# Optimization experiments

Measured on AMD Instinct MI355X. Metric: run time of the kernel, lower is better.

Reference implementation:

```python
import jax, jax.numpy as jnp
import numpy as np

D_MODEL = 14
N_HEADS = 2
SINK_TEMP = 0.1
SINK_ITERS = 20
EPS = 1e-10


def setup_inputs() -> dict:
    key = jax.random.key(0)
    ks = jax.random.split(key, 12)
    b, n, d = 64, 1024, D_MODEL
    s = 1.0 / np.sqrt(d)
    return {
        "x": jax.random.normal(ks[0], (b, n, d), dtype=jnp.float32),
        "certainty": jax.random.uniform(ks[1], (b, n), dtype=jnp.float32),
        "permutation": jax.random.randint(ks[2], (b, n), 0, n).astype(jnp.int64),
        "Wq": jax.random.normal(ks[3], (d, d), dtype=jnp.float32) * s,
        "bq": jnp.zeros((d,), dtype=jnp.float32),
        "Wk": jax.random.normal(ks[4], (d, d), dtype=jnp.float32) * s,
        "bk": jnp.zeros((d,), dtype=jnp.float32),
        "Wv": jax.random.normal(ks[5], (d, d), dtype=jnp.float32) * s,
        "bv": jnp.zeros((d,), dtype=jnp.float32),
        "Wo": jax.random.normal(ks[6], (d, d), dtype=jnp.float32) * s,
        "bo": jnp.zeros((d,), dtype=jnp.float32),
    }


def _split_heads(t, b, n):
    # (b, n, d) -> (b, H, n, hd)
    return t.reshape(b, n, N_HEADS, D_MODEL // N_HEADS).transpose(0, 2, 1, 3)


def reference(x, certainty, permutation, Wq, bq, Wk, bk, Wv, bv, Wo, bo):
    b, n, d = x.shape
    hd = d // N_HEADS
    Q = _split_heads(x @ Wq.T + bq, b, n)
    K = _split_heads(x @ Wk.T + bk, b, n)
    V = _split_heads(x @ Wv.T + bv, b, n)
    scores = jnp.einsum("bhqd,bhkd->bhqk", Q, K) / jnp.sqrt(jnp.float32(hd))
    attn = jax.nn.softmax(scores, axis=-1)  # dropout is identity at eval
    out = jnp.einsum("bhqk,bhkd->bhqd", attn, V)
    out = out.transpose(0, 2, 1, 3).reshape(b, n, d)
    out = out @ Wo.T + bo

    avg_attn = attn.mean(axis=1)  # (b, n, n)
    entropy = -jnp.sum(avg_attn * jnp.log(avg_attn + EPS), axis=-1)  # (b, n)
    max_entropy = jnp.log(jnp.float32(n))
    cert_update = jax.nn.sigmoid(max_entropy - entropy)
    new_certainty = jnp.maximum(certainty, cert_update)

    logits = jnp.log(avg_attn + EPS)
    P = jnp.exp(logits / SINK_TEMP)

    def body(_, P):
        P = P / (P.sum(axis=-1, keepdims=True) + EPS)
        P = P / (P.sum(axis=-2, keepdims=True) + EPS)
        return P

    P = jax.lax.fori_loop(0, SINK_ITERS, body, P)
    new_perm = jnp.argmax(P, axis=-1)  # (b, n)
    new_permutation = jnp.take_along_axis(permutation, new_perm, axis=1)
    return out, new_certainty, new_permutation
```

## Files before the change

kernel.cpp:

```cpp
#include <hip/hip_runtime.h>

#define EPSF    1e-10f
#define MAXENT  6.93147180559945286f
#define SCALEF  0.37796447300922720f

__device__ __forceinline__ float wave_sum(float v) {
#pragma unroll
  for (int off = 32; off > 0; off >>= 1) v += __shfl_xor(v, off);
  return v;
}
__device__ __forceinline__ void wave_sum2(float& a, float& b) {
#pragma unroll
  for (int off = 32; off > 0; off >>= 1) {
    a += __shfl_xor(a, off);
    b += __shfl_xor(b, off);
  }
}
__device__ __forceinline__ void fma4(float a, float4 b, float4& c) {
  c.x = fmaf(a, b.x, c.x); c.y = fmaf(a, b.y, c.y);
  c.z = fmaf(a, b.z, c.z); c.w = fmaf(a, b.w, c.w);
}
__device__ __forceinline__ float dot4(float4 a, float4 b, float acc) {
  acc = fmaf(a.x, b.x, acc); acc = fmaf(a.y, b.y, acc);
  acc = fmaf(a.z, b.z, acc); acc = fmaf(a.w, b.w, acc);
  return acc;
}
__device__ __forceinline__ float4 exp4(float4 s) {
  return make_float4(__expf(s.x), __expf(s.y), __expf(s.z), __expf(s.w));
}
__device__ __forceinline__ float4 cupd(float4 c, float4 v) {
  c.x = fminf(c.x / fmaf(c.x, v.x, EPSF), 1e37f);
  c.y = fminf(c.y / fmaf(c.y, v.y, EPSF), 1e37f);
  c.z = fminf(c.z / fmaf(c.z, v.z, EPSF), 1e37f);
  c.w = fminf(c.w / fmaf(c.w, v.w, EPSF), 1e37f);
  return c;
}
__device__ __forceinline__ float p0e(float s1, float s2, float E1, float E2) {
  float p = fmaf(E1, __expf(s1), fmaf(E2, __expf(s2), EPSF));
  float p2 = p * p, p4 = p2 * p2, p5 = p4 * p;
  return p5 * p5;
}

__global__ __launch_bounds__(256) void qkv_kernel(
    const float* __restrict__ x,
    const float* __restrict__ Wq, const float* __restrict__ bq,
    const float* __restrict__ Wk, const float* __restrict__ bk,
    const float* __restrict__ Wv, const float* __restrict__ bv,
    float* __restrict__ Qt, float* __restrict__ Kt, float* __restrict__ Vt,
    float* __restrict__ R, float* __restrict__ CA, float* __restrict__ CB,
    float* __restrict__ vW) {
  int row = blockIdx.x * 256 + threadIdx.x;
  int b = row >> 10, i = row & 1023;
  float xv[14];
#pragma unroll
  for (int k = 0; k < 14; k++) xv[k] = x[row * 14 + k];
#pragma unroll
  for (int d = 0; d < 14; d++) {
    float q = bq[d], kk = bk[d], vv = bv[d];
#pragma unroll
    for (int k = 0; k < 14; k++) {
      q  = fmaf(xv[k], Wq[d * 14 + k], q);
      kk = fmaf(xv[k], Wk[d * 14 + k], kk);
      vv = fmaf(xv[k], Wv[d * 14 + k], vv);
    }
    int o = b * 14336 + d * 1024 + i;
    Qt[o] = q * SCALEF;
    Kt[o] = kk; Vt[o] = vv;
  }
  R[row] = 1.0f;
  CA[row] = 1.0f;
  CB[row] = 1.0f;
  vW[row] = 0.f;
  vW[row + 65536] = 0.f;
  vW[row + 131072] = 0.f;
  vW[row + 196608] = 0.f;
}

__global__ __launch_bounds__(256, 2) void attn_kernel(
    const float* __restrict__ Qt, const float* __restrict__ Kt, const float* __restrict__ Vt,
    const float* __restrict__ cert_in,
    const float* __restrict__ WoG, const float* __restrict__ boG,
    float* __restrict__ E1o, float* __restrict__ E2o,
    float* __restrict__ out_, float* __restrict__ cert_out) {
  __shared__ float WoS[196];
  __shared__ float boS[14];
  int b = blockIdx.x >> 7;
  int rg = blockIdx.x & 127;
  int tid = threadIdx.x;
  if (tid < 196) WoS[tid] = WoG[tid];
  if (tid < 14) boS[tid] = boG[tid];
  __syncthreads();

  int wave = tid >> 6, lane = tid & 63;
  int i0 = rg * 8 + wave * 2;
  const float4* Ktb = (const float4*)(Kt + b * 14336);
  const float4* Vtb = (const float4*)(Vt + b * 14336);
  float q0[14], q1[14];
#pragma unroll
  for (int d = 0; d < 14; d++) {
    q0[d] = Qt[b * 14336 + d * 1024 + i0];
    q1[d] = Qt[b * 14336 + d * 1024 + i0 + 1];
  }

  float4 e10[4], e20[4], e11[4], e21[4];
  float L10 = 0.f, L20 = 0.f, L11 = 0.f, L21 = 0.f;
  float acc0[14], acc1[14];
#pragma unroll
  for (int d = 0; d < 14; d++) { acc0[d] = 0.f; acc1[d] = 0.f; }
#pragma unroll
  for (int t = 0; t < 4; t++) {
    int g = t * 64 + lane;
    float4 kv[7];
#pragma unroll
    for (int d = 0; d < 7; d++) kv[d] = Ktb[d * 256 + g];
    float4 sa = {0,0,0,0}, sb = {0,0,0,0};
#pragma unroll
    for (int d = 0; d < 7; d++) { fma4(q0[d], kv[d], sa); fma4(q1[d], kv[d], sb); }
    e10[t] = exp4(sa); e11[t] = exp4(sb);
    L10 += e10[t].x + e10[t].y + e10[t].z + e10[t].w;
    L11 += e11[t].x + e11[t].y + e11[t].z + e11[t].w;
#pragma unroll
    for (int d = 0; d < 7; d++) kv[d] = Ktb[(d + 7) * 256 + g];
    sa = make_float4(0,0,0,0); sb = make_float4(0,0,0,0);
#pragma unroll
    for (int d = 0; d < 7; d++) { fma4(q0[d + 7], kv[d], sa); fma4(q1[d + 7], kv[d], sb); }
    e20[t] = exp4(sa); e21[t] = exp4(sb);
    L20 += e20[t].x + e20[t].y + e20[t].z + e20[t].w;
    L21 += e21[t].x + e21[t].y + e21[t].z + e21[t].w;
#pragma unroll
    for (int d = 0; d < 7; d++) {
      float4 vv = Vtb[d * 256 + g];
      acc0[d] += e10[t].x * vv.x + e10[t].y * vv.y + e10[t].z * vv.z + e10[t].w * vv.w;
      acc1[d] += e11[t].x * vv.x + e11[t].y * vv.y + e11[t].z * vv.z + e11[t].w * vv.w;
    }
#pragma unroll
    for (int d = 7; d < 14; d++) {
      float4 vv = Vtb[d * 256 + g];
      acc0[d] += e20[t].x * vv.x + e20[t].y * vv.y + e20[t].z * vv.z + e20[t].w * vv.w;
      acc1[d] += e21[t].x * vv.x + e21[t].y * vv.y + e21[t].z * vv.z + e21[t].w * vv.w;
    }
  }
  wave_sum2(L10, L20); wave_sum2(L11, L21);
  float i10 = 1.0f / L10, i20 = 1.0f / L20, i11 = 1.0f / L11, i21 = 1.0f / L21;

  float ent0 = 0.f, ent1 = 0.f;
#pragma unroll
  for (int t = 0; t < 4; t++) {
    float a;
    a = 0.5f * (e10[t].x * i10 + e20[t].x * i20); ent0 -= a * __logf(a + EPSF);
    a = 0.5f * (e10[t].y * i10 + e20[t].y * i20); ent0 -= a * __logf(a + EPSF);
    a = 0.5f * (e10[t].z * i10 + e20[t].z * i20); ent0 -= a * __logf(a + EPSF);
    a = 0.5f * (e10[t].w * i10 + e20[t].w * i20); ent0 -= a * __logf(a + EPSF);
    a = 0.5f * (e11[t].x * i11 + e21[t].x * i21); ent1 -= a * __logf(a + EPSF);
    a = 0.5f * (e11[t].y * i11 + e21[t].y * i21); ent1 -= a * __logf(a + EPSF);
    a = 0.5f * (e11[t].z * i11 + e21[t].z * i21); ent1 -= a * __logf(a + EPSF);
    a = 0.5f * (e11[t].w * i11 + e21[t].w * i21); ent1 -= a * __logf(a + EPSF);
  }
  wave_sum2(ent0, ent1);
#pragma unroll
  for (int d = 0; d < 14; d += 2) wave_sum2(acc0[d], acc0[d + 1]);
#pragma unroll
  for (int d = 0; d < 14; d += 2) wave_sum2(acc1[d], acc1[d + 1]);

  int row0 = b * 1024 + i0;
  if (lane == 0) {
    E1o[row0] = 0.5f * i10;  E2o[row0] = 0.5f * i20;
    E1o[row0 + 1] = 0.5f * i11; E2o[row0 + 1] = 0.5f * i21;
    cert_out[row0] = fmaxf(cert_in[row0], 1.0f / (1.0f + __expf(ent0 - MAXENT)));
    cert_out[row0 + 1] = fmaxf(cert_in[row0 + 1], 1.0f / (1.0f + __expf(ent1 - MAXENT)));
  }
  if (lane < 14) {
    int d = lane;
    float av0[14], av1[14];
#pragma unroll
    for (int k = 0; k < 14; k++) {
      av0[k] = acc0[k] * (k < 7 ? i10 : i20);
      av1[k] = acc1[k] * (k < 7 ? i11 : i21);
    }
    float s0 = boS[d], s1 = boS[d];
#pragma unroll
    for (int k = 0; k < 14; k++) {
      s0 = fmaf(av0[k], WoS[d * 14 + k], s0);
      s1 = fmaf(av1[k], WoS[d * 14 + k], s1);
    }
    out_[(size_t)row0 * 14 + d] = s0;
    out_[(size_t)(row0 + 1) * 14 + d] = s1;
  }
}


__global__ __launch_bounds__(512) void p0sink1_kernel(
    const float* __restrict__ Qt, const float* __restrict__ Kt,
    const float* __restrict__ E1, const float* __restrict__ E2,
    float* __restrict__ P0, float* __restrict__ R,
    float* __restrict__ vacc, float* __restrict__ vzero, int b0, int G) {
  __shared__ float4 Kl[3584];
  int gb = blockIdx.x >> 5, blk = blockIdx.x & 31;
  int b = b0 + gb;
  int tid = threadIdx.x;
  if (tid < 32) vzero[b * 1024 + blk * 32 + tid] = 0.f;
  const float4* Ktb = (const float4*)(Kt + b * 14336);
  for (int idx = tid; idx < 3584; idx += 512) Kl[idx] = Ktb[idx];
  __syncthreads();

  int wave = tid >> 6, lane = tid & 63;
  int i0 = blk * 32 + wave * 4;
  float q[4][14], e1r[4], e2r[4], u[4];
#pragma unroll
  for (int rr = 0; rr < 4; rr++) {
#pragma unroll
    for (int d = 0; d < 14; d++) q[rr][d] = Qt[b * 14336 + d * 1024 + i0 + rr];
    e1r[rr] = E1[b * 1024 + i0 + rr];
    e2r[rr] = E2[b * 1024 + i0 + rr];
    u[rr] = 0.f;
  }
  float4* P0f4 = (float4*)P0;
#pragma unroll
  for (int t = 0; t < 4; t++) {
    int g = t * 64 + lane;
    float4 kv[14];
#pragma unroll
    for (int d = 0; d < 14; d++) kv[d] = Kl[d * 256 + g];
#pragma unroll
    for (int rr = 0; rr < 4; rr++) {
      float4 s1 = {0,0,0,0}, s2 = {0,0,0,0};
#pragma unroll
      for (int d = 0; d < 7; d++)  fma4(q[rr][d], kv[d], s1);
#pragma unroll
      for (int d = 7; d < 14; d++) fma4(q[rr][d], kv[d], s2);
      float4 pv;
      pv.x = p0e(s1.x, s2.x, e1r[rr], e2r[rr]);
      pv.y = p0e(s1.y, s2.y, e1r[rr], e2r[rr]);
      pv.z = p0e(s1.z, s2.z, e1r[rr], e2r[rr]);
      pv.w = p0e(s1.w, s2.w, e1r[rr], e2r[rr]);
      P0f4[(size_t)(gb * 1024 + i0 + rr) * 256 + g] = pv;
      u[rr] += pv.x; u[rr] += pv.y; u[rr] += pv.z; u[rr] += pv.w;
    }
  }
  wave_sum2(u[0], u[1]); wave_sum2(u[2], u[3]);
  float rv[4];
#pragma unroll
  for (int rr = 0; rr < 4; rr++) {
    float r0 = 1.0f;
    rv[rr] = fminf(r0 / fmaf(r0, u[rr], EPSF), 1e37f);
  }
  if (lane == 0) {
#pragma unroll
    for (int rr = 0; rr < 4; rr++) R[b * 1024 + i0 + rr] = rv[rr];
  }
  int l0 = lane, l1 = 64 + lane, l2 = 128 + lane, l3 = 192 + lane;
  float4 v0 = {0,0,0,0}, v1 = {0,0,0,0}, v2 = {0,0,0,0}, v3 = {0,0,0,0};
  const float4* base = P0f4 + (size_t)(gb * 1024 + i0) * 256;
#pragma unroll
  for (int rr = 0; rr < 4; rr++) {
    const float4* row = base + rr * 256;
    float4 a0 = row[l0], a1 = row[l1], a2 = row[l2], a3 = row[l3];
    fma4(rv[rr], a0, v0); fma4(rv[rr], a1, v1); fma4(rv[rr], a2, v2); fma4(rv[rr], a3, v3);
  }
  __syncthreads();
  float* vbuf = (float*)Kl;
  float4* vb4 = (float4*)vbuf;
  vb4[wave * 256 + l0] = v0; vb4[wave * 256 + l1] = v1;
  vb4[wave * 256 + l2] = v2; vb4[wave * 256 + l3] = v3;
  __syncthreads();
  for (int col = tid; col < 1024; col += 512) {
    float v = 0.f;
#pragma unroll
    for (int w = 0; w < 8; w++) v += vbuf[w * 1024 + col];
    atomicAdd(&vacc[b * 1024 + col], v);
  }
}

__global__ __launch_bounds__(512) void sink_fused(
    const float* __restrict__ P0, const float* __restrict__ Cin,
    float* __restrict__ Cout, float* __restrict__ R,
    const float* __restrict__ vin, float* __restrict__ vacc,
    float* __restrict__ vzero, int b0) {
  __shared__ float vbuf[8192];
  int tid = threadIdx.x;
  int gb = blockIdx.x >> 5, slice = blockIdx.x & 31;
  int b = b0 + gb;

  if (tid < 32) vzero[b * 1024 + slice * 32 + tid] = 0.f;

  int wave = tid >> 6, lane = tid & 63;
  int i0 = slice * 32 + wave * 4;
  int rbase = b * 1024 + i0;
  int l0 = lane, l1 = 64 + lane, l2 = 128 + lane, l3 = 192 + lane;
  const float4* base = (const float4*)P0 + (size_t)(gb * 1024 + i0) * 256;

  float4 a0 = base[l0], a1 = base[l1], a2 = base[l2], a3 = base[l3];
  float4 b0f = base[256 + l0], b1f = base[256 + l1], b2f = base[256 + l2], b3f = base[256 + l3];

  const float4* Cin4 = (const float4*)(Cin + b * 1024);
  const float4* vin4 = (const float4*)(vin + b * 1024);
  float4 c0 = cupd(Cin4[l0], vin4[l0]);
  float4 c1 = cupd(Cin4[l1], vin4[l1]);
  float4 c2 = cupd(Cin4[l2], vin4[l2]);
  float4 c3 = cupd(Cin4[l3], vin4[l3]);
  if (slice == 0 && wave == 0) {
    float4* Co4 = (float4*)(Cout + b * 1024);
    Co4[l0] = c0; Co4[l1] = c1; Co4[l2] = c2; Co4[l3] = c3;
  }

  float rreg[4];
#pragma unroll
  for (int r = 0; r < 4; r++) rreg[r] = R[rbase + r];

  float4 v0 = {0,0,0,0}, v1 = {0,0,0,0}, v2 = {0,0,0,0}, v3 = {0,0,0,0};

#pragma unroll
  for (int r = 0; r < 4; r += 2) {
    float4 na0, na1, na2, na3, nb0, nb1, nb2, nb3;
    if (r + 2 < 4) {
      const float4* nxt = base + (r + 2) * 256;
      na0 = nxt[l0]; na1 = nxt[l1]; na2 = nxt[l2]; na3 = nxt[l3];
      nb0 = nxt[256 + l0]; nb1 = nxt[256 + l1]; nb2 = nxt[256 + l2]; nb3 = nxt[256 + l3];
    }
    float ua = dot4(a3, c3, dot4(a2, c2, dot4(a1, c1, dot4(a0, c0, 0.f))));
    float ub = dot4(b3f, c3, dot4(b2f, c2, dot4(b1f, c1, dot4(b0f, c0, 0.f))));
    wave_sum2(ua, ub);
    float rva = rreg[r], rvb = rreg[r + 1];
    rva = fminf(rva / fmaf(rva, ua, EPSF), 1e37f);
    rvb = fminf(rvb / fmaf(rvb, ub, EPSF), 1e37f);
    if (lane == 0) { R[rbase + r] = rva; R[rbase + r + 1] = rvb; }
    fma4(rva, a0, v0); fma4(rva, a1, v1); fma4(rva, a2, v2); fma4(rva, a3, v3);
    fma4(rvb, b0f, v0); fma4(rvb, b1f, v1); fma4(rvb, b2f, v2); fma4(rvb, b3f, v3);
    if (r + 2 < 4) {
      a0 = na0; a1 = na1; a2 = na2; a3 = na3;
      b0f = nb0; b1f = nb1; b2f = nb2; b3f = nb3;
    }
  }
  float4* vb4 = (float4*)vbuf;
  vb4[wave * 256 + l0] = v0; vb4[wave * 256 + l1] = v1;
  vb4[wave * 256 + l2] = v2; vb4[wave * 256 + l3] = v3;
  __syncthreads();
  for (int col = tid; col < 1024; col += 512) {
    float v = 0.f;
#pragma unroll
    for (int w = 0; w < 8; w++) v += vbuf[w * 1024 + col];
    atomicAdd(&vacc[b * 1024 + col], v);
  }
}

__global__ __launch_bounds__(512) void argmaxP_kernel(
    const float* __restrict__ P0, const float* __restrict__ Cin,
    const float* __restrict__ vfin,
    const int* __restrict__ perm, float* __restrict__ perm_out, int b0) {
  int gb = blockIdx.x >> 7, rg = blockIdx.x & 127;
  int b = b0 + gb;
  int tid = threadIdx.x;
  int wave = tid >> 6, lane = tid & 63;
  int i = rg * 8 + wave;
  const float4* Prow = (const float4*)P0 + (size_t)(gb * 1024 + i) * 256;
  const float4* Cin4 = (const float4*)(Cin + b * 1024);
  const float4* vin4 = (const float4*)(vfin + b * 1024);
  float4 cc[4];
#pragma unroll
  for (int t = 0; t < 4; t++) cc[t] = cupd(Cin4[t * 64 + lane], vin4[t * 64 + lane]);

  float best = -1.0f;
  int bj = 0;
#pragma unroll
  for (int t = 0; t < 4; t++) {
    int g = t * 64 + lane;
    float4 pv = Prow[g], cv = cc[t];
    float val;
    val = pv.x * cv.x; if (val > best) { best = val; bj = 4 * g + 0; }
    val = pv.y * cv.y; if (val > best) { best = val; bj = 4 * g + 1; }
    val = pv.z * cv.z; if (val > best) { best = val; bj = 4 * g + 2; }
    val = pv.w * cv.w; if (val > best) { best = val; bj = 4 * g + 3; }
  }
#pragma unroll
  for (int off = 32; off > 0; off >>= 1) {
    float ob = __shfl_xor(best, off);
    int oj = __shfl_xor(bj, off);
    if (ob > best || (ob == best && oj < bj)) { best = ob; bj = oj; }
  }
  if (lane == 0) perm_out[b * 1024 + i] = (float)perm[b * 1024 + bj];
}


__global__ __launch_bounds__(512) void sinkA_kernel(
    const float* __restrict__ Qt, const float* __restrict__ Kt,
    const float* __restrict__ E1, const float* __restrict__ E2,
    const float* __restrict__ C, float* __restrict__ R) {
  __shared__ float4 Kl[3584];
  int b = blockIdx.x >> 5, blk = blockIdx.x & 31;
  int tid = threadIdx.x;
  const float4* Ktb = (const float4*)(Kt + b * 14336);
  for (int idx = tid; idx < 3584; idx += 512) Kl[idx] = Ktb[idx];
  __syncthreads();
  int wave = tid >> 6, lane = tid & 63;
  int i0 = blk * 32 + wave * 4;
  float q[4][14], e1r[4], e2r[4], u[4];
#pragma unroll
  for (int rr = 0; rr < 4; rr++) {
#pragma unroll
    for (int d = 0; d < 14; d++) q[rr][d] = Qt[b * 14336 + d * 1024 + i0 + rr];
    e1r[rr] = E1[b * 1024 + i0 + rr];
    e2r[rr] = E2[b * 1024 + i0 + rr];
    u[rr] = 0.f;
  }
  const float4* Cb = (const float4*)(C + b * 1024);
#pragma unroll
  for (int t = 0; t < 4; t++) {
    int g = t * 64 + lane;
    float4 kv[14];
#pragma unroll
    for (int d = 0; d < 14; d++) kv[d] = Kl[d * 256 + g];
    float4 cv = Cb[g];
#pragma unroll
    for (int rr = 0; rr < 4; rr++) {
      float4 s1 = {0,0,0,0}, s2 = {0,0,0,0};
#pragma unroll
      for (int d = 0; d < 7; d++)  fma4(q[rr][d], kv[d], s1);
#pragma unroll
      for (int d = 7; d < 14; d++) fma4(q[rr][d], kv[d], s2);
      u[rr] += p0e(s1.x, s2.x, e1r[rr], e2r[rr]) * cv.x;
      u[rr] += p0e(s1.y, s2.y, e1r[rr], e2r[rr]) * cv.y;
      u[rr] += p0e(s1.z, s2.z, e1r[rr], e2r[rr]) * cv.z;
      u[rr] += p0e(s1.w, s2.w, e1r[rr], e2r[rr]) * cv.w;
    }
  }
#pragma unroll
  for (int rr = 0; rr < 4; rr++) u[rr] = wave_sum(u[rr]);
  if (lane == 0) {
#pragma unroll
    for (int rr = 0; rr < 4; rr++) {
      int o = b * 1024 + i0 + rr;
      float rv = R[o];
      R[o] = fminf(rv / fmaf(rv, u[rr], EPSF), 1e37f);
    }
  }
}

__global__ __launch_bounds__(512) void sinkB_kernel(
    const float* __restrict__ Qt, const float* __restrict__ Kt,
    const float* __restrict__ E1, const float* __restrict__ E2,
    const float* __restrict__ R, float* __restrict__ C) {
  __shared__ float4 Ql[3584];
  int b = blockIdx.x >> 5, blk = blockIdx.x & 31;
  int tid = threadIdx.x;
  const float4* Qtb = (const float4*)(Qt + b * 14336);
  for (int idx = tid; idx < 3584; idx += 512) Ql[idx] = Qtb[idx];
  __syncthreads();
  int wave = tid >> 6, lane = tid & 63;
  int j0 = blk * 32 + wave * 4;
  float kk[4][14], v[4];
#pragma unroll
  for (int rr = 0; rr < 4; rr++) {
#pragma unroll
    for (int d = 0; d < 14; d++) kk[rr][d] = Kt[b * 14336 + d * 1024 + j0 + rr];
    v[rr] = 0.f;
  }
  const float4* E1b = (const float4*)(E1 + b * 1024);
  const float4* E2b = (const float4*)(E2 + b * 1024);
  const float4* Rb  = (const float4*)(R + b * 1024);
#pragma unroll
  for (int t = 0; t < 4; t++) {
    int g = t * 64 + lane;
    float4 qv[14];
#pragma unroll
    for (int d = 0; d < 14; d++) qv[d] = Ql[d * 256 + g];
    float4 e1v = E1b[g], e2v = E2b[g], rv = Rb[g];
#pragma unroll
    for (int rr = 0; rr < 4; rr++) {
      float4 s1 = {0,0,0,0}, s2 = {0,0,0,0};
#pragma unroll
      for (int d = 0; d < 7; d++)  fma4(kk[rr][d], qv[d], s1);
#pragma unroll
      for (int d = 7; d < 14; d++) fma4(kk[rr][d], qv[d], s2);
      v[rr] += p0e(s1.x, s2.x, e1v.x, e2v.x) * rv.x;
      v[rr] += p0e(s1.y, s2.y, e1v.y, e2v.y) * rv.y;
      v[rr] += p0e(s1.z, s2.z, e1v.z, e2v.z) * rv.z;
      v[rr] += p0e(s1.w, s2.w, e1v.w, e2v.w) * rv.w;
    }
  }
#pragma unroll
  for (int rr = 0; rr < 4; rr++) v[rr] = wave_sum(v[rr]);
  if (lane == 0) {
#pragma unroll
    for (int rr = 0; rr < 4; rr++) {
      int o = b * 1024 + j0 + rr;
      float cv = C[o];
      C[o] = fminf(cv / fmaf(cv, v[rr], EPSF), 1e37f);
    }
  }
}

__global__ __launch_bounds__(512) void argmax_kernel(
    const float* __restrict__ Qt, const float* __restrict__ Kt,
    const float* __restrict__ E1, const float* __restrict__ E2,
    const float* __restrict__ C, const int* __restrict__ perm,
    float* __restrict__ perm_out) {
  __shared__ float4 Kl[3584];
  int b = blockIdx.x >> 7, rg = blockIdx.x & 127;
  int tid = threadIdx.x;
  const float4* Ktb = (const float4*)(Kt + b * 14336);
  for (int idx = tid; idx < 3584; idx += 512) Kl[idx] = Ktb[idx];
  __syncthreads();
  int wave = tid >> 6, lane = tid & 63;
  int i = rg * 8 + wave;
  int row = b * 1024 + i;
  float q[14];
#pragma unroll
  for (int d = 0; d < 14; d++) q[d] = Qt[b * 14336 + d * 1024 + i];
  float e1r = E1[row], e2r = E2[row];
  const float4* Cb = (const float4*)(C + b * 1024);
  float best = -1.0f;
  int bj = 0;
#pragma unroll
  for (int t = 0; t < 4; t++) {
    int g = t * 64 + lane;
    float4 kv[14];
#pragma unroll
    for (int d = 0; d < 14; d++) kv[d] = Kl[d * 256 + g];
    float4 cv = Cb[g];
    float4 s1 = {0,0,0,0}, s2 = {0,0,0,0};
#pragma unroll
    for (int d = 0; d < 7; d++)  fma4(q[d], kv[d], s1);
#pragma unroll
    for (int d = 7; d < 14; d++) fma4(q[d], kv[d], s2);
    float val;
    val = p0e(s1.x, s2.x, e1r, e2r) * cv.x; if (val > best) { best = val; bj = 4 * g + 0; }
    val = p0e(s1.y, s2.y, e1r, e2r) * cv.y; if (val > best) { best = val; bj = 4 * g + 1; }
    val = p0e(s1.z, s2.z, e1r, e2r) * cv.z; if (val > best) { best = val; bj = 4 * g + 2; }
    val = p0e(s1.w, s2.w, e1r, e2r) * cv.w; if (val > best) { best = val; bj = 4 * g + 3; }
  }
#pragma unroll
  for (int off = 32; off > 0; off >>= 1) {
    float ob = __shfl_xor(best, off);
    int oj = __shfl_xor(bj, off);
    if (ob > best || (ob == best && oj < bj)) { best = ob; bj = oj; }
  }
  if (lane == 0) perm_out[row] = (float)perm[b * 1024 + bj];
}

extern "C" void kernel_launch(void* const* d_in, const int* in_sizes, int n_in,
                              void* d_out, int out_size, void* d_ws, size_t ws_size,
                              hipStream_t stream) {
  const float* x    = (const float*)d_in[0];
  const float* cert = (const float*)d_in[1];
  const int*   perm = (const int*)d_in[2];
  const float* Wq = (const float*)d_in[3];
  const float* bq = (const float*)d_in[4];
  const float* Wk = (const float*)d_in[5];
  const float* bk = (const float*)d_in[6];
  const float* Wv = (const float*)d_in[7];
  const float* bv = (const float*)d_in[8];
  const float* Wo = (const float*)d_in[9];
  const float* bo = (const float*)d_in[10];

  float* out      = (float*)d_out;
  float* cert_out = out + 917504;
  float* perm_out = out + 983040;

  float* ws = (float*)d_ws;
  float* Qt = ws;
  float* Kt = Qt + 917504;
  float* Vt = Kt + 917504;
  float* E1 = Vt + 917504;
  float* E2 = E1 + 65536;
  float* R  = E2 + 65536;
  float* CA = R + 65536;
  float* CB = CA + 65536;
  float* vW = CB + 65536;
  float* P0 = vW + 262144;

  size_t base_f = 3342336u;
  size_t avail_f = (ws_size / 4 > base_f) ? (ws_size / 4 - base_f) : 0;
  size_t perG = 1048576u;
  int G = 0;
  if (avail_f >= 32 * perG) G = 32;
  else if (avail_f >= 16 * perG) G = 16;

  float* Cbuf[2] = {CA, CB};

  qkv_kernel<<<256, 256, 0, stream>>>(x, Wq, bq, Wk, bk, Wv, bv, Qt, Kt, Vt, R, CA, CB, vW);
  attn_kernel<<<8192, 256, 0, stream>>>(Qt, Kt, Vt, cert, Wo, bo, E1, E2, out, cert_out);

  if (G >= 16) {
    for (int b0 = 0; b0 < 64; b0 += G) {
      p0sink1_kernel<<<G * 32, 512, 0, stream>>>(Qt, Kt, E1, E2, P0, R,
          vW + 65536, vW + 3 * 65536, b0, G);
      for (int it = 2; it <= 20; it++) {
        sink_fused<<<G * 32, 512, 0, stream>>>(P0, Cbuf[it & 1], Cbuf[(it + 1) & 1], R,
            vW + (size_t)((it - 1) & 3) * 65536,
            vW + (size_t)(it & 3) * 65536,
            vW + (size_t)((it + 2) & 3) * 65536, b0);
      }
      argmaxP_kernel<<<G * 128, 512, 0, stream>>>(P0, Cbuf[1], vW, perm, perm_out, b0);
    }
  } else {
    for (int it = 0; it < 20; it++) {
      sinkA_kernel<<<2048, 512, 0, stream>>>(Qt, Kt, E1, E2, CA, R);
      sinkB_kernel<<<2048, 512, 0, stream>>>(Qt, Kt, E1, E2, R, CA);
    }
    argmax_kernel<<<8192, 512, 0, stream>>>(Qt, Kt, E1, E2, CA, perm, perm_out);
  }
}
```

Baseline: 1.223 ms.

## Fuse Sinkhorn iterations into one persistent cooperative kernel with grid syncs

Replaces the per-iteration launches (p0sink1, 19 sink_fused, argmaxP per batch group) with a single cooperative kernel. It loops over virtual blocks and separates the phases with grid.sync(), which removes kernel launch gaps and tail effects. Blocks shrink to 256 threads with 8 rows per wave. K is now read directly from global memory instead of being staged in LDS, and the argmax is rewritten inline. The risk is grid-sync overhead, lower per-block parallelism, and a persistent grid sized by occupancy that may be small.

```diff
diff --git a/kernel.cpp b/kernel.cpp
--- a/kernel.cpp
+++ b/kernel.cpp
@@ -1,4 +1,7 @@
 #include <hip/hip_runtime.h>
+#include <hip/hip_cooperative_groups.h>
+
+namespace cg = cooperative_groups;
 
 #define EPSF    1e-10f
 #define MAXENT  6.93147180559945286f
@@ -189,102 +192,106 @@
 }
 
 
-__global__ __launch_bounds__(512) void p0sink1_kernel(
+__device__ __forceinline__ void p0_body(
+    int vb, int b0,
     const float* __restrict__ Qt, const float* __restrict__ Kt,
     const float* __restrict__ E1, const float* __restrict__ E2,
     float* __restrict__ P0, float* __restrict__ R,
-    float* __restrict__ vacc, float* __restrict__ vzero, int b0, int G) {
-  __shared__ float4 Kl[3584];
-  int gb = blockIdx.x >> 5, blk = blockIdx.x & 31;
+    float* __restrict__ vacc, float* __restrict__ vzero, float* vbuf) {
+  int gb = vb >> 5, blk = vb & 31;
   int b = b0 + gb;
   int tid = threadIdx.x;
+  __syncthreads();
   if (tid < 32) vzero[b * 1024 + blk * 32 + tid] = 0.f;
+  int wave = tid >> 6, lane = tid & 63;
+  int i0 = blk * 32 + wave * 8;
   const float4* Ktb = (const float4*)(Kt + b * 14336);
-  for (int idx = tid; idx < 3584; idx += 512) Kl[idx] = Ktb[idx];
-  __syncthreads();
-
-  int wave = tid >> 6, lane = tid & 63;
-  int i0 = blk * 32 + wave * 4;
-  float q[4][14], e1r[4], e2r[4], u[4];
-#pragma unroll
-  for (int rr = 0; rr < 4; rr++) {
-#pragma unroll
-    for (int d = 0; d < 14; d++) q[rr][d] = Qt[b * 14336 + d * 1024 + i0 + rr];
-    e1r[rr] = E1[b * 1024 + i0 + rr];
-    e2r[rr] = E2[b * 1024 + i0 + rr];
-    u[rr] = 0.f;
-  }
   float4* P0f4 = (float4*)P0;
-#pragma unroll
-  for (int t = 0; t < 4; t++) {
-    int g = t * 64 + lane;
-    float4 kv[14];
-#pragma unroll
-    for (int d = 0; d < 14; d++) kv[d] = Kl[d * 256 + g];
-#pragma unroll
-    for (int rr = 0; rr < 4; rr++) {
-      float4 s1 = {0,0,0,0}, s2 = {0,0,0,0};
-#pragma unroll
-      for (int d = 0; d < 7; d++)  fma4(q[rr][d], kv[d], s1);
-#pragma unroll
-      for (int d = 7; d < 14; d++) fma4(q[rr][d], kv[d], s2);
+  float u[8];
+#pragma unroll
+  for (int r = 0; r < 8; r++) u[r] = 0.f;
+#pragma unroll 1
+  for (int ch = 0; ch < 4; ch++) {
+    int ri = i0 + ch * 2;
+    float q0[14], q1[14];
+#pragma unroll
+    for (int d = 0; d < 14; d++) {
+      q0[d] = Qt[b * 14336 + d * 1024 + ri];
+      q1[d] = Qt[b * 14336 + d * 1024 + ri + 1];
+    }
+    float e10 = E1[b * 1024 + ri], e20 = E2[b * 1024 + ri];
+    float e11 = E1[b * 1024 + ri + 1], e21 = E2[b * 1024 + ri + 1];
+#pragma unroll
+    for (int t = 0; t < 4; t++) {
+      int g = t * 64 + lane;
+      float4 kv[7];
+#pragma unroll
+      for (int d = 0; d < 7; d++) kv[d] = Ktb[d * 256 + g];
+      float4 sa = {0,0,0,0}, sb = {0,0,0,0};
+#pragma unroll
+      for (int d = 0; d < 7; d++) { fma4(q0[d], kv[d], sa); fma4(q1[d], kv[d], sb); }
+#pragma unroll
+      for (int d = 0; d < 7; d++) kv[d] = Ktb[(d + 7) * 256 + g];
+      float4 s2a = {0,0,0,0}, s2b = {0,0,0,0};
+#pragma unroll
+      for (int d = 0; d < 7; d++) { fma4(q0[d + 7], kv[d], s2a); fma4(q1[d + 7], kv[d], s2b); }
       float4 pv;
-      pv.x = p0e(s1.x, s2.x, e1r[rr], e2r[rr]);
-      pv.y = p0e(s1.y, s2.y, e1r[rr], e2r[rr]);
-      pv.z = p0e(s1.z, s2.z, e1r[rr], e2r[rr]);
-      pv.w = p0e(s1.w, s2.w, e1r[rr], e2r[rr]);
-      P0f4[(size_t)(gb * 1024 + i0 + rr) * 256 + g] = pv;
-      u[rr] += pv.x; u[rr] += pv.y; u[rr] += pv.z; u[rr] += pv.w;
+      pv.x = p0e(sa.x, s2a.x, e10, e20);
+      pv.y = p0e(sa.y, s2a.y, e10, e20);
+      pv.z = p0e(sa.z, s2a.z, e10, e20);
+      pv.w = p0e(sa.w, s2a.w, e10, e20);
+      P0f4[(size_t)(gb * 1024 + ri) * 256 + g] = pv;
+      u[ch * 2] += pv.x + pv.y + pv.z + pv.w;
+      pv.x = p0e(sb.x, s2b.x, e11, e21);
+      pv.y = p0e(sb.y, s2b.y, e11, e21);
+      pv.z = p0e(sb.z, s2b.z, e11, e21);
+      pv.w = p0e(sb.w, s2b.w, e11, e21);
+      P0f4[(size_t)(gb * 1024 + ri + 1) * 256 + g] = pv;
+      u[ch * 2 + 1] += pv.x + pv.y + pv.z + pv.w;
     }
   }
   wave_sum2(u[0], u[1]); wave_sum2(u[2], u[3]);
-  float rv[4];
-#pragma unroll
-  for (int rr = 0; rr < 4; rr++) {
-    float r0 = 1.0f;
-    rv[rr] = fminf(r0 / fmaf(r0, u[rr], EPSF), 1e37f);
-  }
+  wave_sum2(u[4], u[5]); wave_sum2(u[6], u[7]);
+  float rv[8];
+#pragma unroll
+  for (int r = 0; r < 8; r++)
+    rv[r] = fminf(1.0f / fmaf(1.0f, u[r], EPSF), 1e37f);
   if (lane == 0) {
 #pragma unroll
-    for (int rr = 0; rr < 4; rr++) R[b * 1024 + i0 + rr] = rv[rr];
+    for (int r = 0; r < 8; r++) R[b * 1024 + i0 + r] = rv[r];
   }
   int l0 = lane, l1 = 64 + lane, l2 = 128 + lane, l3 = 192 + lane;
   float4 v0 = {0,0,0,0}, v1 = {0,0,0,0}, v2 = {0,0,0,0}, v3 = {0,0,0,0};
-  const float4* base = P0f4 + (size_t)(gb * 1024 + i0) * 256;
-#pragma unroll
-  for (int rr = 0; rr < 4; rr++) {
-    const float4* row = base + rr * 256;
-    float4 a0 = row[l0], a1 = row[l1], a2 = row[l2], a3 = row[l3];
-    fma4(rv[rr], a0, v0); fma4(rv[rr], a1, v1); fma4(rv[rr], a2, v2); fma4(rv[rr], a3, v3);
-  }
-  __syncthreads();
-  float* vbuf = (float*)Kl;
+  const float4* basep = P0f4 + (size_t)(gb * 1024 + i0) * 256;
+#pragma unroll 1
+  for (int r = 0; r < 8; r++) {
+    const float4* row = basep + r * 256;
+    fma4(rv[r], row[l0], v0); fma4(rv[r], row[l1], v1);
+    fma4(rv[r], row[l2], v2); fma4(rv[r], row[l3], v3);
+  }
   float4* vb4 = (float4*)vbuf;
   vb4[wave * 256 + l0] = v0; vb4[wave * 256 + l1] = v1;
   vb4[wave * 256 + l2] = v2; vb4[wave * 256 + l3] = v3;
   __syncthreads();
-  for (int col = tid; col < 1024; col += 512) {
-    float v = 0.f;
-#pragma unroll
-    for (int w = 0; w < 8; w++) v += vbuf[w * 1024 + col];
+  for (int col = tid; col < 1024; col += 256) {
+    float v = vbuf[col] + vbuf[1024 + col] + vbuf[2048 + col] + vbuf[3072 + col];
     atomicAdd(&vacc[b * 1024 + col], v);
   }
 }
 
-__global__ __launch_bounds__(512) void sink_fused(
+__device__ __forceinline__ void sink_body(
+    int vb, int b0,
     const float* __restrict__ P0, const float* __restrict__ Cin,
     float* __restrict__ Cout, float* __restrict__ R,
     const float* __restrict__ vin, float* __restrict__ vacc,
-    float* __restrict__ vzero, int b0) {
-  __shared__ float vbuf[8192];
-  int tid = threadIdx.x;
-  int gb = blockIdx.x >> 5, slice = blockIdx.x & 31;
+    float* __restrict__ vzero, float* vbuf) {
+  int gb = vb >> 5, slice = vb & 31;
   int b = b0 + gb;
-
+  int tid = threadIdx.x;
+  __syncthreads();
   if (tid < 32) vzero[b * 1024 + slice * 32 + tid] = 0.f;
-
-  int wave = tid >> 6, lane = tid & 63;
-  int i0 = slice * 32 + wave * 4;
+  int wave = tid >> 6, lane = tid & 63;
+  int i0 = slice * 32 + wave * 8;
   int rbase = b * 1024 + i0;
   int l0 = lane, l1 = 64 + lane, l2 = 128 + lane, l3 = 192 + lane;
   const float4* base = (const float4*)P0 + (size_t)(gb * 1024 + i0) * 256;
@@ -302,13 +309,230 @@
     float4* Co4 = (float4*)(Cout + b * 1024);
     Co4[l0] = c0; Co4[l1] = c1; Co4[l2] = c2; Co4[l3] = c3;
   }
+  float rreg[8];
+#pragma unroll
+  for (int r = 0; r < 8; r++) rreg[r] = R[rbase + r];
+
+  float4 v0 = {0,0,0,0}, v1 = {0,0,0,0}, v2 = {0,0,0,0}, v3 = {0,0,0,0};
+#pragma unroll
+  for (int r = 0; r < 8; r += 2) {
+    float4 na0, na1, na2, na3, nb0, nb1, nb2, nb3;
+    if (r + 2 < 8) {
+      const float4* nxt = base + (r + 2) * 256;
+      na0 = nxt[l0]; na1 = nxt[l1]; na2 = nxt[l2]; na3 = nxt[l3];
+      nb0 = nxt[256 + l0]; nb1 = nxt[256 + l1]; nb2 = nxt[256 + l2]; nb3 = nxt[256 + l3];
+    }
+    float ua = dot4(a3, c3, dot4(a2, c2, dot4(a1, c1, dot4(a0, c0, 0.f))));
+    float ub = dot4(b3f, c3, dot4(b2f, c2, dot4(b1f, c1, dot4(b0f, c0, 0.f))));
+    wave_sum2(ua, ub);
+    float rva = rreg[r], rvb = rreg[r + 1];
+    rva = fminf(rva / fmaf(rva, ua, EPSF), 1e37f);
+    rvb = fminf(rvb / fmaf(rvb, ub, EPSF), 1e37f);
+    if (lane == 0) { R[rbase + r] = rva; R[rbase + r + 1] = rvb; }
+    fma4(rva, a0, v0); fma4(rva, a1, v1); fma4(rva, a2, v2); fma4(rva, a3, v3);
+    fma4(rvb, b0f, v0); fma4(rvb, b1f, v1); fma4(rvb, b2f, v2); fma4(rvb, b3f, v3);
+    if (r + 2 < 8) {
+      a0 = na0; a1 = na1; a2 = na2; a3 = na3;
+      b0f = nb0; b1f = nb1; b2f = nb2; b3f = nb3;
+    }
+  }
+  float4* vb4 = (float4*)vbuf;
+  vb4[wave * 256 + l0] = v0; vb4[wave * 256 + l1] = v1;
+  vb4[wave * 256 + l2] = v2; vb4[wave * 256 + l3] = v3;
+  __syncthreads();
+  for (int col = tid; col < 1024; col += 256) {
+    float v = vbuf[col] + vbuf[1024 + col] + vbuf[2048 + col] + vbuf[3072 + col];
+    atomicAdd(&vacc[b * 1024 + col], v);
+  }
+}
+
+__device__ __forceinline__ void argmax_body(
+    int vb, int b0,
+    const float* __restrict__ P0, const float* __restrict__ Cin,
+    const float* __restrict__ vfin,
+    const int* __restrict__ perm, float* __restrict__ perm_out) {
+  int gb = vb >> 5, blk = vb & 31;
+  int b = b0 + gb;
+  int tid = threadIdx.x;
+  int wave = tid >> 6, lane = tid & 63;
+  int i0 = blk * 32 + wave * 8;
+  const float4* Cin4 = (const float4*)(Cin + b * 1024);
+  const float4* vin4 = (const float4*)(vfin + b * 1024);
+  float4 cc[4];
+#pragma unroll
+  for (int t = 0; t < 4; t++) cc[t] = cupd(Cin4[t * 64 + lane], vin4[t * 64 + lane]);
+#pragma unroll 1
+  for (int r = 0; r < 8; r++) {
+    int i = i0 + r;
+    const float4* Prow = (const float4*)P0 + (size_t)(gb * 1024 + i) * 256;
+    float best = -1.0f;
+    int bj = 0;
+#pragma unroll
+    for (int t = 0; t < 4; t++) {
+      int g = t * 64 + lane;
+      float4 pv = Prow[g], cv = cc[t];
+      float val;
+      val = pv.x * cv.x; if (val > best) { best = val; bj = 4 * g + 0; }
+      val = pv.y * cv.y; if (val > best) { best = val; bj = 4 * g + 1; }
+      val = pv.z * cv.z; if (val > best) { best = val; bj = 4 * g + 2; }
+      val = pv.w * cv.w; if (val > best) { best = val; bj = 4 * g + 3; }
+    }
+#pragma unroll
+    for (int off = 32; off > 0; off >>= 1) {
+      float ob = __shfl_xor(best, off);
+      int oj = __shfl_xor(bj, off);
+      if (ob > best || (ob == best && oj < bj)) { best = ob; bj = oj; }
+    }
+    if (lane == 0) perm_out[b * 1024 + i] = (float)perm[b * 1024 + bj];
+  }
+}
+
+__global__ __launch_bounds__(256) void sink_coop(
+    const float* __restrict__ Qt, const float* __restrict__ Kt,
+    const float* __restrict__ E1, const float* __restrict__ E2,
+    float* __restrict__ P0, float* __restrict__ R,
+    float* __restrict__ CA, float* __restrict__ CB, float* __restrict__ vW,
+    const int* __restrict__ perm, float* __restrict__ perm_out) {
+  __shared__ float vbuf[4096];
+  cg::grid_group grid = cg::this_grid();
+  for (int b0 = 0; b0 < 64; b0 += 32) {
+    for (int vb = blockIdx.x; vb < 1024; vb += gridDim.x)
+      p0_body(vb, b0, Qt, Kt, E1, E2, P0, R, vW + 65536, vW + 3 * 65536, vbuf);
+    grid.sync();
+    for (int it = 2; it <= 20; ++it) {
+      const float* Cin = (it & 1) ? CB : CA;
+      float* Cout = (it & 1) ? CA : CB;
+      for (int vb = blockIdx.x; vb < 1024; vb += gridDim.x)
+        sink_body(vb, b0, P0, Cin, Cout, R,
+                  vW + (size_t)((it - 1) & 3) * 65536,
+                  vW + (size_t)(it & 3) * 65536,
+                  vW + (size_t)((it + 2) & 3) * 65536, vbuf);
+      grid.sync();
+    }
+    for (int vb = blockIdx.x; vb < 1024; vb += gridDim.x)
+      argmax_body(vb, b0, P0, CB, vW, perm, perm_out);
+    grid.sync();
+  }
+}
+
+
+__global__ __launch_bounds__(512) void p0sink1_kernel(
+    const float* __restrict__ Qt, const float* __restrict__ Kt,
+    const float* __restrict__ E1, const float* __restrict__ E2,
+    float* __restrict__ P0, float* __restrict__ R,
+    float* __restrict__ vacc, float* __restrict__ vzero, int b0, int G) {
+  __shared__ float4 Kl[3584];
+  int gb = blockIdx.x >> 5, blk = blockIdx.x & 31;
+  int b = b0 + gb;
+  int tid = threadIdx.x;
+  if (tid < 32) vzero[b * 1024 + blk * 32 + tid] = 0.f;
+  const float4* Ktb = (const float4*)(Kt + b * 14336);
+  for (int idx = tid; idx < 3584; idx += 512) Kl[idx] = Ktb[idx];
+  __syncthreads();
+
+  int wave = tid >> 6, lane = tid & 63;
+  int i0 = blk * 32 + wave * 4;
+  float q[4][14], e1r[4], e2r[4], u[4];
+#pragma unroll
+  for (int rr = 0; rr < 4; rr++) {
+#pragma unroll
+    for (int d = 0; d < 14; d++) q[rr][d] = Qt[b * 14336 + d * 1024 + i0 + rr];
+    e1r[rr] = E1[b * 1024 + i0 + rr];
+    e2r[rr] = E2[b * 1024 + i0 + rr];
+    u[rr] = 0.f;
+  }
+  float4* P0f4 = (float4*)P0;
+#pragma unroll
+  for (int t = 0; t < 4; t++) {
+    int g = t * 64 + lane;
+    float4 kv[14];
+#pragma unroll
+    for (int d = 0; d < 14; d++) kv[d] = Kl[d * 256 + g];
+#pragma unroll
+    for (int rr = 0; rr < 4; rr++) {
+      float4 s1 = {0,0,0,0}, s2 = {0,0,0,0};
+#pragma unroll
+      for (int d = 0; d < 7; d++)  fma4(q[rr][d], kv[d], s1);
+#pragma unroll
+      for (int d = 7; d < 14; d++) fma4(q[rr][d], kv[d], s2);
+      float4 pv;
+      pv.x = p0e(s1.x, s2.x, e1r[rr], e2r[rr]);
+      pv.y = p0e(s1.y, s2.y, e1r[rr], e2r[rr]);
+      pv.z = p0e(s1.z, s2.z, e1r[rr], e2r[rr]);
+      pv.w = p0e(s1.w, s2.w, e1r[rr], e2r[rr]);
+      P0f4[(size_t)(gb * 1024 + i0 + rr) * 256 + g] = pv;
+      u[rr] += pv.x; u[rr] += pv.y; u[rr] += pv.z; u[rr] += pv.w;
+    }
+  }
+  wave_sum2(u[0], u[1]); wave_sum2(u[2], u[3]);
+  float rv[4];
+#pragma unroll
+  for (int rr = 0; rr < 4; rr++)
+    rv[rr] = fminf(1.0f / fmaf(1.0f, u[rr], EPSF), 1e37f);
+  if (lane == 0) {
+#pragma unroll
+    for (int rr = 0; rr < 4; rr++) R[b * 1024 + i0 + rr] = rv[rr];
+  }
+  int l0 = lane, l1 = 64 + lane, l2 = 128 + lane, l3 = 192 + lane;
+  float4 v0 = {0,0,0,0}, v1 = {0,0,0,0}, v2 = {0,0,0,0}, v3 = {0,0,0,0};
+  const float4* base = P0f4 + (size_t)(gb * 1024 + i0) * 256;
+#pragma unroll
+  for (int rr = 0; rr < 4; rr++) {
+    const float4* row = base + rr * 256;
+    fma4(rv[rr], row[l0], v0); fma4(rv[rr], row[l1], v1);
+    fma4(rv[rr], row[l2], v2); fma4(rv[rr], row[l3], v3);
+  }
+  __syncthreads();
+  float* vbuf = (float*)Kl;
+  float4* vb4 = (float4*)vbuf;
+  vb4[wave * 256 + l0] = v0; vb4[wave * 256 + l1] = v1;
+  vb4[wave * 256 + l2] = v2; vb4[wave * 256 + l3] = v3;
+  __syncthreads();
+  for (int col = tid; col < 1024; col += 512) {
+    float v = 0.f;
+#pragma unroll
+    for (int w = 0; w < 8; w++) v += vbuf[w * 1024 + col];
+    atomicAdd(&vacc[b * 1024 + col], v);
+  }
+}
+
+__global__ __launch_bounds__(512) void sink_fused(
+    const float* __restrict__ P0, const float* __restrict__ Cin,
+    float* __restrict__ Cout, float* __restrict__ R,
+    const float* __restrict__ vin, float* __restrict__ vacc,
+    float* __restrict__ vzero, int b0) {
+  __shared__ float vbuf[8192];
+  int tid = threadIdx.x;
+  int gb = blockIdx.x >> 5, slice = blockIdx.x & 31;
+  int b = b0 + gb;
+
+  if (tid < 32) vzero[b * 1024 + slice * 32 + tid] = 0.f;
+
+  int wave = tid >> 6, lane = tid & 63;
+  int i0 = slice * 32 + wave * 4;
+  int rbase = b * 1024 + i0;
+  int l0 = lane, l1 = 64 + lane, l2 = 128 + lane, l3 = 192 + lane;
+  const float4* base = (const float4*)P0 + (size_t)(gb * 1024 + i0) * 256;
+
+  float4 a0 = base[l0], a1 = base[l1], a2 = base[l2], a3 = base[l3];
+  float4 b0f = base[256 + l0], b1f = base[256 + l1], b2f = base[256 + l2], b3f = base[256 + l3];
+
+  const float4* Cin4 = (const float4*)(Cin + b * 1024);
+  const float4* vin4 = (const float4*)(vin + b * 1024);
+  float4 c0 = cupd(Cin4[l0], vin4[l0]);
+  float4 c1 = cupd(Cin4[l1], vin4[l1]);
+  float4 c2 = cupd(Cin4[l2], vin4[l2]);
+  float4 c3 = cupd(Cin4[l3], vin4[l3]);
+  if (slice == 0 && wave == 0) {
+    float4* Co4 = (float4*)(Cout + b * 1024);
+    Co4[l0] = c0; Co4[l1] = c1; Co4[l2] = c2; Co4[l3] = c3;
+  }
 
   float rreg[4];
 #pragma unroll
   for (int r = 0; r < 4; r++) rreg[r] = R[rbase + r];
 
   float4 v0 = {0,0,0,0}, v1 = {0,0,0,0}, v2 = {0,0,0,0}, v3 = {0,0,0,0};
-
 #pragma unroll
   for (int r = 0; r < 4; r += 2) {
     float4 na0, na1, na2, na3, nb0, nb1, nb2, nb3;
@@ -575,12 +799,40 @@
   if (avail_f >= 32 * perG) G = 32;
   else if (avail_f >= 16 * perG) G = 16;
 
+  static int coopGrid = -2;
+  if (coopGrid == -2) {
+    int dev = 0;
+    hipGetDevice(&dev);
+    int supported = 0;
+    hipDeviceGetAttribute(&supported, hipDeviceAttributeCooperativeLaunch, dev);
+    int nCU = 0;
+    hipDeviceGetAttribute(&nCU, hipDeviceAttributeMultiprocessorCount, dev);
+    int maxB = 0;
+    hipError_t oe = hipOccupancyMaxActiveBlocksPerMultiprocessor(
+        &maxB, reinterpret_cast<const void*>(&sink_coop), 256, 0);
+    int cap = (oe == hipSuccess) ? maxB * nCU : 0;
+    coopGrid = (supported && cap >= 256) ? (cap < 1024 ? cap : 1024) : 0;
+  }
+
   float* Cbuf[2] = {CA, CB};
 
   qkv_kernel<<<256, 256, 0, stream>>>(x, Wq, bq, Wk, bk, Wv, bv, Qt, Kt, Vt, R, CA, CB, vW);
   attn_kernel<<<8192, 256, 0, stream>>>(Qt, Kt, Vt, cert, Wo, bo, E1, E2, out, cert_out);
 
-  if (G >= 16) {
+  bool done = false;
+  if (G >= 32 && coopGrid > 0) {
+    void* args[] = {
+      (void*)&Qt, (void*)&Kt, (void*)&E1, (void*)&E2, (void*)&P0, (void*)&R,
+      (void*)&CA, (void*)&CB, (void*)&vW, (void*)&perm, (void*)&perm_out
+    };
+    hipError_t e = hipLaunchCooperativeKernel(
+        reinterpret_cast<const void*>(&sink_coop),
+        dim3(coopGrid), dim3(256), args, 0, stream);
+    if (e == hipSuccess) done = true;
+    else coopGrid = 0;
+  }
+
+  if (!done && G >= 16) {
     for (int b0 = 0; b0 < 64; b0 += G) {
       p0sink1_kernel<<<G * 32, 512, 0, stream>>>(Qt, Kt, E1, E2, P0, R,
           vW + 65536, vW + 3 * 65536, b0, G);
@@ -592,7 +844,10 @@
       }
       argmaxP_kernel<<<G * 128, 512, 0, stream>>>(P0, Cbuf[1], vW, perm, perm_out, b0);
     }
-  } else {
+    done = true;
+  }
+
+  if (!done) {
     for (int it = 0; it < 20; it++) {
       sinkA_kernel<<<2048, 512, 0, stream>>>(Qt, Kt, E1, E2, CA, R);
       sinkB_kernel<<<2048, 512, 0, stream>>>(Qt, Kt, E1, E2, R, CA);
```

New measurement: 1.226 ms. Within noise of the previous version (+0.3%).
